# Performance work log

Measured on AMD Instinct MI355X. Metric: run time of the kernel, lower is better.

The kernel has to match this reference:

```python
import jax, jax.numpy as jnp
import numpy as np

T, D, F, V = 16384, 1024, 2048, 4096


def _mlp(x, w1, w2):
    # residual ReLU MLP stand-in for a transformer stack (tokenwise)
    return x + jax.nn.relu(x @ w1) @ w2


def setup_inputs() -> dict:
    key = jax.random.key(0)
    ks = jax.random.split(key, 11)
    s1 = 1.0 / np.sqrt(D)
    s2 = 1.0 / np.sqrt(F)
    g = lambda k, shape, sc: jax.random.normal(k, shape, dtype=jnp.float32) * sc
    return {
        "inputs_embeds": g(ks[0], (T, D), 1.0),
        "enc_w1": g(ks[1], (D, F), s1),
        "enc_w2": g(ks[2], (F, D), s2),
        "back_w1": g(ks[3], (D, F), s1),
        "back_w2": g(ks[4], (F, D), s2),
        "dec_w1": g(ks[5], (D, F), s1),
        "dec_w2": g(ks[6], (F, D), s2),
        "sp_w": g(ks[7], (D, 1), s1),
        "sp_b": jnp.zeros((1,), jnp.float32),
        "pos_emb": g(ks[8], (T, D), 0.02),
        "lm_head": g(ks[9], (D, V), s1),
        "cu_seq_lens": jnp.array([0, 4096, 8192, 12288, 16384], dtype=jnp.int32),
    }


def reference(inputs_embeds, enc_w1, enc_w2, back_w1, back_w2, dec_w1, dec_w2,
              sp_w, sp_b, pos_emb, lm_head, cu_seq_lens):
    # --- encoder (3-layer stack stand-in) ---
    enc = _mlp(inputs_embeds, enc_w1, enc_w2)                 # [T, D]
    # --- token gate: sigmoid + threshold ---
    w = jax.nn.sigmoid(enc @ sp_w + sp_b)[:, 0]               # [T]
    mask = w >= 0.5                                           # keep mask (= ~zero_mask)
    mi = mask.astype(jnp.int32)
    # --- ragged re-pack: within-segment rank of kept tokens (new position ids) ---
    ecs = jnp.cumsum(mi) - mi                                 # exclusive cumsum of kept
    seg = jnp.searchsorted(cu_seq_lens[1:], jnp.arange(T), side="right")
    base = ecs[cu_seq_lens[:-1]][seg]                         # kept-count before each segment
    new_pos = ecs - base                                      # arange(length) per new segment
    # stable sort places kept tokens first in original (packed) order,
    # exactly matching the per-segment concat of the torch version
    order = jnp.argsort(jnp.logical_not(mask), stable=True)   # [T]
    valid = mask[order]
    # gather + weight by gate value, add new position embedding
    gathered = (enc * w[:, None])[order] + pos_emb[new_pos[order]]
    gathered = jnp.where(valid[:, None], gathered, 0.0)
    # --- backbone compute on packed kept tokens ---
    bb = _mlp(gathered, back_w1, back_w2)                     # [T, D] (padded tail unused)
    # --- scatter-combine: kept slots <- backbone, dropped slots <- encoder residual ---
    inv = jnp.argsort(order)
    combined = jnp.where(mask[:, None], bb[inv], enc)         # [T, D]
    # --- decoder (3-layer stack stand-in) + lm head ---
    dec = _mlp(combined, dec_w1, dec_w2)
    logits = dec @ lm_head                                    # [T, V] fp32
    return logits
```

## Files before the change

### kernel.cpp

```cpp
#include <hip/hip_runtime.h>
#include <hip/hip_bf16.h>
#include <math.h>

static constexpr int TT = 16384;
static constexpr int DD = 1024;
static constexpr int FF = 2048;
static constexpr int VV = 4096;
static constexpr int CAP = 4096;
#define TAU 0.02f

using bf16 = __hip_bfloat16;
typedef __attribute__((ext_vector_type(8))) short bf16x8;
typedef __attribute__((ext_vector_type(4))) float f32x4;

__device__ inline void gload16(const void* g, void* l) {
    __builtin_amdgcn_global_load_lds(
        (const __attribute__((address_space(1))) void*)g,
        (__attribute__((address_space(3))) void*)l, 16, 0, 0);
}

template<int EPI , bool WB16, bool WF32, bool ROWLIM, bool GPART>
__global__ __launch_bounds__(512, 2)
void mgemm8(const bf16* __restrict__ A, const bf16* __restrict__ BT,
            const float* __restrict__ X, bf16* __restrict__ Ob,
            float* __restrict__ Of, float* __restrict__ gpart,
            const float* __restrict__ qv,
            int M, int N, int K, const int* __restrict__ rowlim)
{
    if constexpr (ROWLIM) { if ((int)blockIdx.y * 256 >= *rowlim) return; }
    const int m0 = blockIdx.y * 256, n0 = blockIdx.x * 256;

    extern __shared__ char smem[];

    const int tid = threadIdx.x;
    const int wv = tid >> 6, ln = tid & 63;
    const int wm = wv >> 2, wn = wv & 3;
    const int lr = ln & 15, lk = ln >> 4;
    const int swz = (lr & 7) << 4;

    const bf16* Ag = A  + (size_t)m0 * K;
    const bf16* Bg = BT + (size_t)n0 * K;

    const int NT = K >> 6;
    const int NI = NT >> 1;

    const int aoff0 = (wm * 128 + lr) * 128;
    const int boff0 = 32768 + (wn * 64 + lr) * 128;
    const int cb0 = (lk * 16) ^ swz;
    const int cb1 = (64 + lk * 16) ^ swz;

    auto STAGE = [&](const bf16* g, int h, int kt, int buf, int op) {
        const int r = ln >> 3;
        const int c = ((ln & 7) ^ r) * 8;
        const bf16* s = g + (size_t)(h * 128 + wv * 16 + r) * K + kt * 64 + c;
        char* d = smem + buf * 65536 + op * 32768 + h * 16384 + wv * 2048;
        gload16(s, d);
        gload16(s + (size_t)8 * K, d + 1024);
    };
    auto stage_j = [&](int j) {
        const int tile = j >> 2;
        if (tile >= NT) return;
        const int part = j & 3;
        const int buf = tile & 1;
        if (part < 2) STAGE(Bg, part, tile, buf, 1);
        else          STAGE(Ag, part - 2, tile, buf, 0);
    };

    bf16x8 afr[2][2], bfr[4][2];
    f32x4 acc[8][4];
    #pragma unroll
    for (int m = 0; m < 8; ++m)
        #pragma unroll
        for (int n = 0; n < 4; ++n) acc[m][n] = (f32x4){0.f, 0.f, 0.f, 0.f};

#define DS_A(BUF, Q) do {                                                     \
    const char* _p = smem + (BUF) * 65536 + aoff0 + (Q) * 4096;               \
    afr[0][0] = *(const bf16x8*)(_p + cb0);                                   \
    afr[0][1] = *(const bf16x8*)(_p + cb1);                                   \
    afr[1][0] = *(const bf16x8*)(_p + 2048 + cb0);                            \
    afr[1][1] = *(const bf16x8*)(_p + 2048 + cb1);                            \
} while (0)

#define DS_B(BUF) do {                                                        \
    const char* _p = smem + (BUF) * 65536 + boff0;                            \
    _Pragma("unroll")                                                         \
    for (int nf = 0; nf < 4; ++nf) {                                          \
        bfr[nf][0] = *(const bf16x8*)(_p + nf * 2048 + cb0);                  \
        bfr[nf][1] = *(const bf16x8*)(_p + nf * 2048 + cb1);                  \
    }                                                                         \
} while (0)

#define MFMAQ(Q) do {                                                         \
    __builtin_amdgcn_s_setprio(1);                                            \
    _Pragma("unroll")                                                         \
    for (int m2 = 0; m2 < 2; ++m2)                                            \
        _Pragma("unroll")                                                     \
        for (int nf = 0; nf < 4; ++nf) {                                      \
            acc[(Q) * 2 + m2][nf] = __builtin_amdgcn_mfma_f32_16x16x32_bf16(  \
                afr[m2][0], bfr[nf][0], acc[(Q) * 2 + m2][nf], 0, 0, 0);      \
            acc[(Q) * 2 + m2][nf] = __builtin_amdgcn_mfma_f32_16x16x32_bf16(  \
                afr[m2][1], bfr[nf][1], acc[(Q) * 2 + m2][nf], 0, 0, 0);      \
        }                                                                     \
    __builtin_amdgcn_s_setprio(0);                                            \
} while (0)

#define PHASE(Q, BUF, DOB, J, W)                                              \
    {                                                                         \
        DS_A(BUF, Q);                                                         \
        if (DOB) DS_B(BUF);                                                   \
        stage_j(J);                                                           \
        if ((W) == 1)      asm volatile("s_waitcnt vmcnt(6)" ::: "memory");   \
        else if ((W) == 2) asm volatile("s_waitcnt vmcnt(0)" ::: "memory");   \
        __builtin_amdgcn_sched_barrier(0);                                    \
        __builtin_amdgcn_s_barrier();                                         \
        MFMAQ(Q);                                                             \
        __builtin_amdgcn_s_barrier();                                         \
    }

    STAGE(Bg, 0, 0, 0, 1); STAGE(Bg, 1, 0, 0, 1);
    STAGE(Ag, 0, 0, 0, 0); STAGE(Ag, 1, 0, 0, 0);
    asm volatile("s_waitcnt vmcnt(4)" ::: "memory");
    STAGE(Bg, 0, 1, 1, 1); STAGE(Bg, 1, 1, 1, 1);
    STAGE(Ag, 0, 1, 1, 0);
    asm volatile("s_waitcnt vmcnt(6)" ::: "memory");
    __builtin_amdgcn_sched_barrier(0);
    __builtin_amdgcn_s_barrier();

    for (int i = 0; i < NI; ++i) {
        const int jb = 7 + 8 * i;
        const bool last = (i + 1 == NI);
        PHASE(0, 0, true,  jb + 0, 0);
        PHASE(1, 0, false, jb + 1, 0);
        PHASE(2, 0, false, jb + 2, 0);
        PHASE(3, 0, false, jb + 3, last ? 2 : 1);
        PHASE(0, 1, true,  jb + 4, 0);
        PHASE(1, 1, false, jb + 5, 0);
        PHASE(2, 1, false, jb + 6, 0);
        PHASE(3, 1, false, jb + 7, last ? 0 : 1);
    }

#undef PHASE
#undef MFMAQ
#undef DS_B
#undef DS_A

    if constexpr (GPART) {
        float qvv[4];
        #pragma unroll
        for (int nf = 0; nf < 4; ++nf) qvv[nf] = qv[n0 + wn * 64 + nf * 16 + lr];
        #pragma unroll
        for (int mf = 0; mf < 8; ++mf)
            #pragma unroll
            for (int rr = 0; rr < 4; ++rr) {
                float s = 0.f;
                #pragma unroll
                for (int nf = 0; nf < 4; ++nf) s += fmaxf(acc[mf][nf][rr], 0.f) * qvv[nf];
                s += __shfl_xor(s, 1, 64); s += __shfl_xor(s, 2, 64);
                s += __shfl_xor(s, 4, 64); s += __shfl_xor(s, 8, 64);
                if (lr == 0)
                    gpart[(size_t)(blockIdx.x * 4 + wn) * M +
                          (m0 + wm * 128 + mf * 16 + lk * 4 + rr)] = s;
            }
    }

    #pragma unroll
    for (int mf = 0; mf < 8; ++mf)
        #pragma unroll
        for (int nf = 0; nf < 4; ++nf)
            #pragma unroll
            for (int rr = 0; rr < 4; ++rr) {
                const int row = m0 + wm * 128 + mf * 16 + lk * 4 + rr;
                const int col = n0 + wn * 64 + nf * 16 + lr;
                float v = acc[mf][nf][rr];
                if constexpr (EPI == 1) v = fmaxf(v, 0.f);
                if constexpr (EPI == 2) v += X[(size_t)row * N + col];
                if constexpr (WB16) Ob[(size_t)row * N + col] = __float2bfloat16(v);
                if constexpr (WF32) Of[(size_t)row * N + col] = v;
            }
}

__global__ void wtrans(const float* __restrict__ W, bf16* __restrict__ Th,
                       int R, int C)
{
    __shared__ float tile[32][33];
    const int tx = threadIdx.x & 31, ty = threadIdx.x >> 5;
    const int rb = blockIdx.y * 32, cb = blockIdx.x * 32;
    #pragma unroll
    for (int i = 0; i < 32; i += 8)
        tile[ty + i][tx] = W[(size_t)(rb + ty + i) * C + cb + tx];
    __syncthreads();
    #pragma unroll
    for (int i = 0; i < 32; i += 8)
        Th[(size_t)(cb + ty + i) * R + rb + tx] = __float2bfloat16(tile[tx][ty + i]);
}

__global__ void castx(const float* __restrict__ x, bf16* __restrict__ xb)
{
    const int i = blockIdx.x * 256 + threadIdx.x;
    const float4 v = ((const float4*)x)[i];
    xb[i * 4 + 0] = __float2bfloat16(v.x);
    xb[i * 4 + 1] = __float2bfloat16(v.y);
    xb[i * 4 + 2] = __float2bfloat16(v.z);
    xb[i * 4 + 3] = __float2bfloat16(v.w);
}

__global__ void qvec(const float* __restrict__ w2, const float* __restrict__ sp,
                     float* __restrict__ q)
{
    const int f  = blockIdx.x * 4 + (threadIdx.x >> 6);
    const int ln = threadIdx.x & 63;
    float s = 0.f;
    const float* row = w2 + (size_t)f * DD;
    for (int k = ln; k < DD; k += 64) s += row[k] * sp[k];
    #pragma unroll
    for (int off = 32; off > 0; off >>= 1) s += __shfl_xor(s, off, 64);
    if (ln == 0) q[f] = s;
}

__global__ void gate2(const float* __restrict__ x, const float* __restrict__ spw,
                      const float* __restrict__ spb, const float* __restrict__ gpart,
                      float* __restrict__ w, int* __restrict__ mi,
                      float* __restrict__ sx, int* __restrict__ flags,
                      int* __restrict__ cnt)
{
    const int t  = blockIdx.x * 4 + (threadIdx.x >> 6);
    const int ln = threadIdx.x & 63;
    float s = 0.f;
    const float* row = x + (size_t)t * DD;
    for (int k = ln; k < DD; k += 64) s += row[k] * spw[k];
    #pragma unroll
    for (int off = 32; off > 0; off >>= 1) s += __shfl_xor(s, off, 64);
    float g = (ln < 32) ? gpart[(size_t)ln * TT + t] : 0.f;
    #pragma unroll
    for (int off = 32; off > 0; off >>= 1) g += __shfl_xor(g, off, 64);
    if (ln == 0) {
        const float logit = s + g + spb[0];
        const float sg = 1.f / (1.f + expf(-logit));
        w[t]  = sg;
        mi[t] = (sg >= 0.5f) ? 1 : 0;
        sx[t] = s;
        if (fabsf(logit) < TAU) {
            const int i = atomicAdd(cnt, 1);
            if (i < CAP) flags[i] = t;
        }
    }
}

__global__ void fixgemv(const float* __restrict__ x, const float* __restrict__ w1,
                        const float* __restrict__ qv, const int* __restrict__ flags,
                        const int* __restrict__ cnt, float* __restrict__ gpf)
{
    const int nb = min(*cnt, CAP);
    const int t0 = blockIdx.y * 16;
    if (t0 >= nb) return;
    const int ntk = min(16, nb - t0);
    const int f = blockIdx.x * 256 + threadIdx.x;
    const float qf = qv[f];
    __shared__ float xs[16][64];
    __shared__ float red[4][16];
    float acc[16];
    #pragma unroll
    for (int tk = 0; tk < 16; ++tk) acc[tk] = 0.f;

    for (int d0 = 0; d0 < DD; d0 += 64) {
        __syncthreads();
        for (int i = threadIdx.x; i < 16 * 64; i += 256) {
            const int tk = i >> 6, dd = i & 63;
            xs[tk][dd] = (tk < ntk)
                ? x[(size_t)flags[t0 + tk] * DD + d0 + dd] : 0.f;
        }
        __syncthreads();
        for (int dd = 0; dd < 64; ++dd) {
            const float wv = w1[(size_t)(d0 + dd) * FF + f];
            #pragma unroll
            for (int tk = 0; tk < 16; ++tk) acc[tk] += xs[tk][dd] * wv;
        }
    }
    const int wv_ = threadIdx.x >> 6, ln = threadIdx.x & 63;
    #pragma unroll
    for (int tk = 0; tk < 16; ++tk) {
        float v = fmaxf(acc[tk], 0.f) * qf;
        #pragma unroll
        for (int off = 32; off > 0; off >>= 1) v += __shfl_xor(v, off, 64);
        if (ln == 0) red[wv_][tk] = v;
    }
    __syncthreads();
    if (threadIdx.x < 16)
        gpf[(size_t)blockIdx.x * CAP + t0 + threadIdx.x] =
            red[0][threadIdx.x] + red[1][threadIdx.x] +
            red[2][threadIdx.x] + red[3][threadIdx.x];
}

__global__ void fixres(const float* __restrict__ sx, const float* __restrict__ spb,
                       const float* __restrict__ gpf, const int* __restrict__ flags,
                       const int* __restrict__ cnt, float* __restrict__ w,
                       int* __restrict__ mi)
{
    const int nb = min(*cnt, CAP);
    for (int i = blockIdx.x * 256 + threadIdx.x; i < nb; i += gridDim.x * 256) {
        const int t = flags[i];
        float s = sx[t] + spb[0];
        #pragma unroll
        for (int fc = 0; fc < 8; ++fc) s += gpf[(size_t)fc * CAP + i];
        const float sg = 1.f / (1.f + expf(-s));
        w[t]  = sg;
        mi[t] = (sg >= 0.5f) ? 1 : 0;
    }
}

__global__ void scan_kernel(const int* __restrict__ mi, const int* __restrict__ cu,
                            int* __restrict__ ecs, int* __restrict__ meta)
{
    __shared__ int sums[256];
    const int tid  = threadIdx.x;
    const int base = tid * 64;
    int s = 0;
    for (int i = 0; i < 64; ++i) s += mi[base + i];
    sums[tid] = s;
    __syncthreads();
    for (int off = 1; off < 256; off <<= 1) {
        int v = (tid >= off) ? sums[tid - off] : 0;
        __syncthreads();
        sums[tid] += v;
        __syncthreads();
    }
    int run = (tid == 0) ? 0 : sums[tid - 1];
    for (int i = 0; i < 64; ++i) { ecs[base + i] = run; run += mi[base + i]; }
    if (tid == 255) meta[0] = sums[255];
    if (tid < 4) {
        const int idx = cu[tid];
        const int tc = idx >> 6, rem = idx & 63;
        int e = (tc == 0) ? 0 : sums[tc - 1];
        for (int i = 0; i < rem; ++i) e += mi[tc * 64 + i];
        meta[1 + tid] = e;
    }
}

__global__ void pack_kernel(const float* __restrict__ enc, const float* __restrict__ w,
                            const int* __restrict__ mi, const int* __restrict__ ecs,
                            const int* __restrict__ cu, const int* __restrict__ meta,
                            const float* __restrict__ pos_emb,
                            float* __restrict__ Pf, bf16* __restrict__ Pb)
{
    const int t    = blockIdx.x * 4 + (threadIdx.x >> 6);
    const int lane = threadIdx.x & 63;
    if (!mi[t]) return;
    const int e = ecs[t];
    int seg = 0;
    #pragma unroll
    for (int ss = 1; ss < 4; ++ss) if (t >= cu[ss]) seg = ss;
    const int np = e - meta[1 + seg];
    const float wt = w[t];
    const float4* src = (const float4*)(enc + (size_t)t * DD);
    const float4* pe  = (const float4*)(pos_emb + (size_t)np * DD);
    float4* dstf = (float4*)(Pf + (size_t)e * DD);
    bf16*   dstb = Pb + (size_t)e * DD;
    for (int c = lane; c < DD / 4; c += 64) {
        float4 v = src[c], p = pe[c];
        v.x = v.x * wt + p.x; v.y = v.y * wt + p.y;
        v.z = v.z * wt + p.z; v.w = v.w * wt + p.w;
        dstf[c] = v;
        dstb[c * 4 + 0] = __float2bfloat16(v.x);
        dstb[c * 4 + 1] = __float2bfloat16(v.y);
        dstb[c * 4 + 2] = __float2bfloat16(v.z);
        dstb[c * 4 + 3] = __float2bfloat16(v.w);
    }
}

__global__ void combine_kernel(float* __restrict__ ENC, const float* __restrict__ BBf,
                               const int* __restrict__ mi, const int* __restrict__ ecs,
                               bf16* __restrict__ Cb)
{
    const int t    = blockIdx.x * 4 + (threadIdx.x >> 6);
    const int lane = threadIdx.x & 63;
    const bool kept = mi[t] != 0;
    const float4* src = kept ? (const float4*)(BBf + (size_t)ecs[t] * DD)
                             : (const float4*)(ENC + (size_t)t * DD);
    float4* dstf = (float4*)(ENC + (size_t)t * DD);
    bf16*   dstb = Cb + (size_t)t * DD;
    for (int c = lane; c < DD / 4; c += 64) {
        const float4 v = src[c];
        if (kept) dstf[c] = v;
        dstb[c * 4 + 0] = __float2bfloat16(v.x);
        dstb[c * 4 + 1] = __float2bfloat16(v.y);
        dstb[c * 4 + 2] = __float2bfloat16(v.z);
        dstb[c * 4 + 3] = __float2bfloat16(v.w);
    }
}

extern "C" void kernel_launch(void* const* d_in, const int* in_sizes, int n_in,
                              void* d_out, int out_size, void* d_ws, size_t ws_size,
                              hipStream_t stream)
{
    (void)in_sizes; (void)n_in; (void)out_size; (void)ws_size;
    const float* x   = (const float*)d_in[0];
    const float* ew1 = (const float*)d_in[1];
    const float* ew2 = (const float*)d_in[2];
    const float* bw1 = (const float*)d_in[3];
    const float* bw2 = (const float*)d_in[4];
    const float* dw1 = (const float*)d_in[5];
    const float* dw2 = (const float*)d_in[6];
    const float* spw = (const float*)d_in[7];
    const float* spb = (const float*)d_in[8];
    const float* pem = (const float*)d_in[9];
    const float* lmh = (const float*)d_in[10];
    const int*   cu  = (const int*)d_in[11];
    float* out = (float*)d_out;

    (void)hipFuncSetAttribute((const void*)mgemm8<1, true, false, false, true>,
                              hipFuncAttributeMaxDynamicSharedMemorySize, 131072);
    (void)hipFuncSetAttribute((const void*)mgemm8<2, false, true, false, false>,
                              hipFuncAttributeMaxDynamicSharedMemorySize, 131072);
    (void)hipFuncSetAttribute((const void*)mgemm8<1, true, false, true, false>,
                              hipFuncAttributeMaxDynamicSharedMemorySize, 131072);
    (void)hipFuncSetAttribute((const void*)mgemm8<2, false, true, true, false>,
                              hipFuncAttributeMaxDynamicSharedMemorySize, 131072);
    (void)hipFuncSetAttribute((const void*)mgemm8<1, true, false, false, false>,
                              hipFuncAttributeMaxDynamicSharedMemorySize, 131072);
    (void)hipFuncSetAttribute((const void*)mgemm8<2, true, false, false, false>,
                              hipFuncAttributeMaxDynamicSharedMemorySize, 131072);
    (void)hipFuncSetAttribute((const void*)mgemm8<0, false, true, false, false>,
                              hipFuncAttributeMaxDynamicSharedMemorySize, 131072);

    char* w = (char*)d_ws;
    auto alloc = [&](size_t bytes) { char* p = w; w += bytes; return p; };
    bf16* ew1T = (bf16*)alloc((size_t)FF * DD * 2);
    bf16* ew2T = (bf16*)alloc((size_t)DD * FF * 2);
    bf16* bw1T = (bf16*)alloc((size_t)FF * DD * 2);
    bf16* bw2T = (bf16*)alloc((size_t)DD * FF * 2);
    bf16* dw1T = (bf16*)alloc((size_t)FF * DD * 2);
    bf16* dw2T = (bf16*)alloc((size_t)DD * FF * 2);
    bf16* lmhT = (bf16*)alloc((size_t)VV * DD * 2);
    float* qv  = (float*)alloc((size_t)FF * 4);
    float* GP  = (float*)alloc((size_t)32 * TT * 4);
    float* WG  = (float*)alloc((size_t)TT * 4);
    int*  MI   = (int*)alloc((size_t)TT * 4);
    int*  ECS  = (int*)alloc((size_t)TT * 4);
    int*  META = (int*)alloc(64);
    float* SX  = (float*)alloc((size_t)TT * 4);
    int*  FLAGS= (int*)alloc((size_t)CAP * 4);
    int*  CNT  = (int*)alloc(64);
    float* GPF = (float*)alloc((size_t)8 * CAP * 4);
    bf16* Xb   = (bf16*)alloc((size_t)TT * DD * 2);
    bf16* Hb   = (bf16*)alloc((size_t)TT * FF * 2);
    float* ENC = (float*)alloc((size_t)TT * DD * 4);
    float* Pf  = (float*)alloc((size_t)TT * DD * 4);
    bf16* Pb   = (bf16*)alloc((size_t)TT * DD * 2);
    bf16* Cb   = Xb;
    bf16* DECb = Pb;

    const dim3 blk(256);
    const dim3 blk8(512);

    (void)hipMemsetAsync(CNT, 0, 4, stream);

    castx<<<TT * DD / 4 / 256, blk, 0, stream>>>(x, Xb);
    wtrans<<<dim3(FF / 32, DD / 32), blk, 0, stream>>>(ew1, ew1T, DD, FF);
    wtrans<<<dim3(DD / 32, FF / 32), blk, 0, stream>>>(ew2, ew2T, FF, DD);
    wtrans<<<dim3(FF / 32, DD / 32), blk, 0, stream>>>(bw1, bw1T, DD, FF);
    wtrans<<<dim3(DD / 32, FF / 32), blk, 0, stream>>>(bw2, bw2T, FF, DD);
    wtrans<<<dim3(FF / 32, DD / 32), blk, 0, stream>>>(dw1, dw1T, DD, FF);
    wtrans<<<dim3(DD / 32, FF / 32), blk, 0, stream>>>(dw2, dw2T, FF, DD);
    wtrans<<<dim3(VV / 32, DD / 32), blk, 0, stream>>>(lmh, lmhT, DD, VV);
    qvec<<<FF / 4, blk, 0, stream>>>(ew2, spw, qv);

    mgemm8<1, true, false, false, true><<<dim3(FF / 256, TT / 256), blk8, 131072, stream>>>(
        Xb, ew1T, nullptr, Hb, nullptr, GP, qv, TT, FF, DD, nullptr);

    gate2<<<TT / 4, blk, 0, stream>>>(x, spw, spb, GP, WG, MI, SX, FLAGS, CNT);
    fixgemv<<<dim3(8, CAP / 16), blk, 0, stream>>>(x, ew1, qv, FLAGS, CNT, GPF);
    fixres<<<16, blk, 0, stream>>>(SX, spb, GPF, FLAGS, CNT, WG, MI);
    scan_kernel<<<1, blk, 0, stream>>>(MI, cu, ECS, META);

    mgemm8<2, false, true, false, false><<<dim3(DD / 256, TT / 256), blk8, 131072, stream>>>(
        Hb, ew2T, x, nullptr, ENC, nullptr, nullptr, TT, DD, FF, nullptr);

    pack_kernel<<<TT / 4, blk, 0, stream>>>(ENC, WG, MI, ECS, cu, META, pem, Pf, Pb);

    mgemm8<1, true, false, true, false><<<dim3(FF / 256, TT / 256), blk8, 131072, stream>>>(
        Pb, bw1T, nullptr, Hb, nullptr, nullptr, nullptr, TT, FF, DD, META);
    mgemm8<2, false, true, true, false><<<dim3(DD / 256, TT / 256), blk8, 131072, stream>>>(
        Hb, bw2T, Pf, nullptr, Pf, nullptr, nullptr, TT, DD, FF, META);

    combine_kernel<<<TT / 4, blk, 0, stream>>>(ENC, Pf, MI, ECS, Cb);

    mgemm8<1, true, false, false, false><<<dim3(FF / 256, TT / 256), blk8, 131072, stream>>>(
        Cb, dw1T, nullptr, Hb, nullptr, nullptr, nullptr, TT, FF, DD, nullptr);
    mgemm8<2, true, false, false, false><<<dim3(DD / 256, TT / 256), blk8, 131072, stream>>>(
        Hb, dw2T, ENC, DECb, nullptr, nullptr, nullptr, TT, DD, FF, nullptr);

    mgemm8<0, false, true, false, false><<<dim3(VV / 256, TT / 256), blk8, 131072, stream>>>(
        DECb, lmhT, nullptr, nullptr, out, nullptr, nullptr, TT, VV, DD, nullptr);
}
```

Measured before the change: 860.8 us.

## Fuse weight transposes, fold gate dot into cast, split fixup GEMV over D

Merges the seven weight-transpose launches into one kernel, and folds the x·sp_w dot product into the fp32-to-bf16 cast so the gate kernel no longer rereads x. The fp32 recheck of near-threshold tokens is restructured: a D-split partial-H kernel with 32 tokens per block writes partials into the Pf buffer, and a separate reducer applies ReLU, q and the sigmoid. The cap on flagged tokens drops from 4096 to 1024. This cuts launch count and redundant reads of x and w1, but if more than 1024 tokens fall near the threshold the rest keep the bf16-based gate decision.

```diff
diff --git a/kernel.cpp b/kernel.cpp
--- a/kernel.cpp
+++ b/kernel.cpp
@@ -6,7 +6,7 @@
 static constexpr int DD = 1024;
 static constexpr int FF = 2048;
 static constexpr int VV = 4096;
-static constexpr int CAP = 4096;
+static constexpr int CAP = 1024;
 #define TAU 0.02f
 
 using bf16 = __hip_bfloat16;
@@ -179,29 +179,69 @@
             }
 }
 
-__global__ void wtrans(const float* __restrict__ W, bf16* __restrict__ Th,
-                       int R, int C)
-{
+__global__ void wtrans_all(const float* __restrict__ e1, const float* __restrict__ e2,
+                           const float* __restrict__ b1, const float* __restrict__ b2,
+                           const float* __restrict__ d1, const float* __restrict__ d2,
+                           const float* __restrict__ lm,
+                           bf16* __restrict__ e1T, bf16* __restrict__ e2T,
+                           bf16* __restrict__ b1T, bf16* __restrict__ b2T,
+                           bf16* __restrict__ d1T, bf16* __restrict__ d2T,
+                           bf16* __restrict__ lmT)
+{
+    int bid = blockIdx.x;
+    const float* W; bf16* T; int R, C;
+    if (bid < 12288) {
+        const int m = bid >> 11;
+        bid &= 2047;
+        R = (m & 1) ? FF : DD;
+        C = (m & 1) ? DD : FF;
+        switch (m) {
+            case 0:  W = e1; T = e1T; break;
+            case 1:  W = e2; T = e2T; break;
+            case 2:  W = b1; T = b1T; break;
+            case 3:  W = b2; T = b2T; break;
+            case 4:  W = d1; T = d1T; break;
+            default: W = d2; T = d2T; break;
+        }
+    } else {
+        bid -= 12288; W = lm; T = lmT; R = DD; C = VV;
+    }
+    const int tc = C >> 5;
+    const int cb = (bid % tc) * 32, rb = (bid / tc) * 32;
+
     __shared__ float tile[32][33];
     const int tx = threadIdx.x & 31, ty = threadIdx.x >> 5;
-    const int rb = blockIdx.y * 32, cb = blockIdx.x * 32;
     #pragma unroll
     for (int i = 0; i < 32; i += 8)
         tile[ty + i][tx] = W[(size_t)(rb + ty + i) * C + cb + tx];
     __syncthreads();
     #pragma unroll
     for (int i = 0; i < 32; i += 8)
-        Th[(size_t)(cb + ty + i) * R + rb + tx] = __float2bfloat16(tile[tx][ty + i]);
-}
-
-__global__ void castx(const float* __restrict__ x, bf16* __restrict__ xb)
-{
-    const int i = blockIdx.x * 256 + threadIdx.x;
-    const float4 v = ((const float4*)x)[i];
-    xb[i * 4 + 0] = __float2bfloat16(v.x);
-    xb[i * 4 + 1] = __float2bfloat16(v.y);
-    xb[i * 4 + 2] = __float2bfloat16(v.z);
-    xb[i * 4 + 3] = __float2bfloat16(v.w);
+        T[(size_t)(cb + ty + i) * R + rb + tx] = __float2bfloat16(tile[tx][ty + i]);
+}
+
+__global__ void castx2(const float* __restrict__ x, const float* __restrict__ spw,
+                       bf16* __restrict__ xb, float* __restrict__ sx)
+{
+    const int t  = blockIdx.x * 4 + (threadIdx.x >> 6);
+    const int ln = threadIdx.x & 63;
+    const float4* row = (const float4*)(x + (size_t)t * DD);
+    const float4* sp4 = (const float4*)spw;
+    bf16* dst = xb + (size_t)t * DD;
+    float s = 0.f;
+    #pragma unroll
+    for (int q = 0; q < 4; ++q) {
+        const int c = q * 64 + ln;
+        const float4 v = row[c], p = sp4[c];
+        s += v.x * p.x + v.y * p.y + v.z * p.z + v.w * p.w;
+        dst[c * 4 + 0] = __float2bfloat16(v.x);
+        dst[c * 4 + 1] = __float2bfloat16(v.y);
+        dst[c * 4 + 2] = __float2bfloat16(v.z);
+        dst[c * 4 + 3] = __float2bfloat16(v.w);
+    }
+    #pragma unroll
+    for (int off = 32; off > 0; off >>= 1) s += __shfl_xor(s, off, 64);
+    if (ln == 0) sx[t] = s;
 }
 
 __global__ void qvec(const float* __restrict__ w2, const float* __restrict__ sp,
@@ -217,92 +257,81 @@
     if (ln == 0) q[f] = s;
 }
 
-__global__ void gate2(const float* __restrict__ x, const float* __restrict__ spw,
-                      const float* __restrict__ spb, const float* __restrict__ gpart,
-                      float* __restrict__ w, int* __restrict__ mi,
-                      float* __restrict__ sx, int* __restrict__ flags,
+__global__ void gate2(const float* __restrict__ sx, const float* __restrict__ spb,
+                      const float* __restrict__ gpart, float* __restrict__ w,
+                      int* __restrict__ mi, int* __restrict__ flags,
                       int* __restrict__ cnt)
 {
-    const int t  = blockIdx.x * 4 + (threadIdx.x >> 6);
+    const int t = blockIdx.x * 256 + threadIdx.x;
+    float s = sx[t] + spb[0];
+    #pragma unroll
+    for (int j = 0; j < 32; ++j) s += gpart[(size_t)j * TT + t];
+    const float sg = 1.f / (1.f + expf(-s));
+    w[t]  = sg;
+    mi[t] = (sg >= 0.5f) ? 1 : 0;
+    if (fabsf(s) < TAU) {
+        const int i = atomicAdd(cnt, 1);
+        if (i < CAP) flags[i] = t;
+    }
+}
+
+__global__ __launch_bounds__(256)
+void fixh(const float* __restrict__ x, const float* __restrict__ w1,
+          const int* __restrict__ flags, const int* __restrict__ cnt,
+          float* __restrict__ Hpart)
+{
+    const int nb = min(*cnt, CAP);
+    const int t0 = blockIdx.z * 32;
+    if (t0 >= nb) return;
+    const int ntk = min(32, nb - t0);
+    const int f  = blockIdx.x * 256 + threadIdx.x;
+    const int d0 = blockIdx.y * 256;
+
+    __shared__ float xs[32][256];
+    for (int i = threadIdx.x; i < 32 * 64; i += 256) {
+        const int tk = i >> 6, dq = i & 63;
+        float4 v = (tk < ntk)
+            ? *(const float4*)&x[(size_t)flags[t0 + tk] * DD + d0 + dq * 4]
+            : make_float4(0.f, 0.f, 0.f, 0.f);
+        *(float4*)&xs[tk][dq * 4] = v;
+    }
+    __syncthreads();
+
+    float acc[32];
+    #pragma unroll
+    for (int tk = 0; tk < 32; ++tk) acc[tk] = 0.f;
+    for (int dd = 0; dd < 256; ++dd) {
+        const float wv = w1[(size_t)(d0 + dd) * FF + f];
+        #pragma unroll
+        for (int tk = 0; tk < 32; ++tk) acc[tk] += xs[tk][dd] * wv;
+    }
+    for (int tk = 0; tk < ntk; ++tk)
+        Hpart[((size_t)blockIdx.y * CAP + (t0 + tk)) * FF + f] = acc[tk];
+}
+
+__global__ void fixres2(const float* __restrict__ sx, const float* __restrict__ spb,
+                        const float* __restrict__ Hpart, const float* __restrict__ qv,
+                        const int* __restrict__ flags, const int* __restrict__ cnt,
+                        float* __restrict__ w, int* __restrict__ mi)
+{
+    const int nb = min(*cnt, CAP);
+    const int i  = blockIdx.x * 4 + (threadIdx.x >> 6);
     const int ln = threadIdx.x & 63;
+    if (i >= nb) return;
     float s = 0.f;
-    const float* row = x + (size_t)t * DD;
-    for (int k = ln; k < DD; k += 64) s += row[k] * spw[k];
+    for (int f = ln; f < FF; f += 64) {
+        const float h = Hpart[(size_t)(0 * CAP + i) * FF + f]
+                      + Hpart[(size_t)(1 * CAP + i) * FF + f]
+                      + Hpart[(size_t)(2 * CAP + i) * FF + f]
+                      + Hpart[(size_t)(3 * CAP + i) * FF + f];
+        s += fmaxf(h, 0.f) * qv[f];
+    }
     #pragma unroll
     for (int off = 32; off > 0; off >>= 1) s += __shfl_xor(s, off, 64);
-    float g = (ln < 32) ? gpart[(size_t)ln * TT + t] : 0.f;
-    #pragma unroll
-    for (int off = 32; off > 0; off >>= 1) g += __shfl_xor(g, off, 64);
     if (ln == 0) {
-        const float logit = s + g + spb[0];
+        const int t = flags[i];
+        const float logit = sx[t] + s + spb[0];
         const float sg = 1.f / (1.f + expf(-logit));
-        w[t]  = sg;
-        mi[t] = (sg >= 0.5f) ? 1 : 0;
-        sx[t] = s;
-        if (fabsf(logit) < TAU) {
-            const int i = atomicAdd(cnt, 1);
-            if (i < CAP) flags[i] = t;
-        }
-    }
-}
-
-__global__ void fixgemv(const float* __restrict__ x, const float* __restrict__ w1,
-                        const float* __restrict__ qv, const int* __restrict__ flags,
-                        const int* __restrict__ cnt, float* __restrict__ gpf)
-{
-    const int nb = min(*cnt, CAP);
-    const int t0 = blockIdx.y * 16;
-    if (t0 >= nb) return;
-    const int ntk = min(16, nb - t0);
-    const int f = blockIdx.x * 256 + threadIdx.x;
-    const float qf = qv[f];
-    __shared__ float xs[16][64];
-    __shared__ float red[4][16];
-    float acc[16];
-    #pragma unroll
-    for (int tk = 0; tk < 16; ++tk) acc[tk] = 0.f;
-
-    for (int d0 = 0; d0 < DD; d0 += 64) {
-        __syncthreads();
-        for (int i = threadIdx.x; i < 16 * 64; i += 256) {
-            const int tk = i >> 6, dd = i & 63;
-            xs[tk][dd] = (tk < ntk)
-                ? x[(size_t)flags[t0 + tk] * DD + d0 + dd] : 0.f;
-        }
-        __syncthreads();
-        for (int dd = 0; dd < 64; ++dd) {
-            const float wv = w1[(size_t)(d0 + dd) * FF + f];
-            #pragma unroll
-            for (int tk = 0; tk < 16; ++tk) acc[tk] += xs[tk][dd] * wv;
-        }
-    }
-    const int wv_ = threadIdx.x >> 6, ln = threadIdx.x & 63;
-    #pragma unroll
-    for (int tk = 0; tk < 16; ++tk) {
-        float v = fmaxf(acc[tk], 0.f) * qf;
-        #pragma unroll
-        for (int off = 32; off > 0; off >>= 1) v += __shfl_xor(v, off, 64);
-        if (ln == 0) red[wv_][tk] = v;
-    }
-    __syncthreads();
-    if (threadIdx.x < 16)
-        gpf[(size_t)blockIdx.x * CAP + t0 + threadIdx.x] =
-            red[0][threadIdx.x] + red[1][threadIdx.x] +
-            red[2][threadIdx.x] + red[3][threadIdx.x];
-}
-
-__global__ void fixres(const float* __restrict__ sx, const float* __restrict__ spb,
-                       const float* __restrict__ gpf, const int* __restrict__ flags,
-                       const int* __restrict__ cnt, float* __restrict__ w,
-                       int* __restrict__ mi)
-{
-    const int nb = min(*cnt, CAP);
-    for (int i = blockIdx.x * 256 + threadIdx.x; i < nb; i += gridDim.x * 256) {
-        const int t = flags[i];
-        float s = sx[t] + spb[0];
-        #pragma unroll
-        for (int fc = 0; fc < 8; ++fc) s += gpf[(size_t)fc * CAP + i];
-        const float sg = 1.f / (1.f + expf(-s));
         w[t]  = sg;
         mi[t] = (sg >= 0.5f) ? 1 : 0;
     }
@@ -440,7 +469,6 @@
     float* SX  = (float*)alloc((size_t)TT * 4);
     int*  FLAGS= (int*)alloc((size_t)CAP * 4);
     int*  CNT  = (int*)alloc(64);
-    float* GPF = (float*)alloc((size_t)8 * CAP * 4);
     bf16* Xb   = (bf16*)alloc((size_t)TT * DD * 2);
     bf16* Hb   = (bf16*)alloc((size_t)TT * FF * 2);
     float* ENC = (float*)alloc((size_t)TT * DD * 4);
@@ -448,28 +476,24 @@
     bf16* Pb   = (bf16*)alloc((size_t)TT * DD * 2);
     bf16* Cb   = Xb;
     bf16* DECb = Pb;
+    float* Hpart = Pf;
 
     const dim3 blk(256);
     const dim3 blk8(512);
 
     (void)hipMemsetAsync(CNT, 0, 4, stream);
 
-    castx<<<TT * DD / 4 / 256, blk, 0, stream>>>(x, Xb);
-    wtrans<<<dim3(FF / 32, DD / 32), blk, 0, stream>>>(ew1, ew1T, DD, FF);
-    wtrans<<<dim3(DD / 32, FF / 32), blk, 0, stream>>>(ew2, ew2T, FF, DD);
-    wtrans<<<dim3(FF / 32, DD / 32), blk, 0, stream>>>(bw1, bw1T, DD, FF);
-    wtrans<<<dim3(DD / 32, FF / 32), blk, 0, stream>>>(bw2, bw2T, FF, DD);
-    wtrans<<<dim3(FF / 32, DD / 32), blk, 0, stream>>>(dw1, dw1T, DD, FF);
-    wtrans<<<dim3(DD / 32, FF / 32), blk, 0, stream>>>(dw2, dw2T, FF, DD);
-    wtrans<<<dim3(VV / 32, DD / 32), blk, 0, stream>>>(lmh, lmhT, DD, VV);
+    castx2<<<TT / 4, blk, 0, stream>>>(x, spw, Xb, SX);
+    wtrans_all<<<16384, blk, 0, stream>>>(ew1, ew2, bw1, bw2, dw1, dw2, lmh,
+                                          ew1T, ew2T, bw1T, bw2T, dw1T, dw2T, lmhT);
     qvec<<<FF / 4, blk, 0, stream>>>(ew2, spw, qv);
 
     mgemm8<1, true, false, false, true><<<dim3(FF / 256, TT / 256), blk8, 131072, stream>>>(
         Xb, ew1T, nullptr, Hb, nullptr, GP, qv, TT, FF, DD, nullptr);
 
-    gate2<<<TT / 4, blk, 0, stream>>>(x, spw, spb, GP, WG, MI, SX, FLAGS, CNT);
-    fixgemv<<<dim3(8, CAP / 16), blk, 0, stream>>>(x, ew1, qv, FLAGS, CNT, GPF);
-    fixres<<<16, blk, 0, stream>>>(SX, spb, GPF, FLAGS, CNT, WG, MI);
+    gate2<<<TT / 256, blk, 0, stream>>>(SX, spb, GP, WG, MI, FLAGS, CNT);
+    fixh<<<dim3(FF / 256, 4, CAP / 32), blk, 0, stream>>>(x, ew1, FLAGS, CNT, Hpart);
+    fixres2<<<CAP / 4, blk, 0, stream>>>(SX, spb, Hpart, qv, FLAGS, CNT, WG, MI);
     scan_kernel<<<1, blk, 0, stream>>>(MI, cu, ECS, META);
 
     mgemm8<2, false, true, false, false><<<dim3(DD / 256, TT / 256), blk8, 131072, stream>>>(
```

New measurement: 765.7 us. 1.12x faster.
